# Kernel tuning notes

Measured on AMD Instinct MI355X. Metric: run time of the kernel, lower is better.

The kernel has to match this reference:

```python
import jax, jax.numpy as jnp
import numpy as np

N_NODES = 100000
N_EDGES = 3200000
IN_F, HID, OUT = 24, 64, 1


def _gcn_conv(x, W, b, src, dst, norm, n):
    # x: [N, Fin] -> h: [N, Fout]; PyG GCNConv: lin first, then normalized aggregation, then bias
    h = x @ W                                    # [N, Fout]
    msg = h[src] * norm[:, None]                 # [E+N, Fout] gathered, norm-weighted messages
    agg = jax.ops.segment_sum(msg, dst, num_segments=n)  # scatter-add to targets
    return agg + b


def setup_inputs() -> dict:
    key = jax.random.key(0)
    k1, k2, k3, k4 = jax.random.split(key, 4)
    x = jax.random.normal(k1, (N_NODES, IN_F), dtype=jnp.float32)
    edge_index = jax.random.randint(k2, (2, N_EDGES), 0, N_NODES, dtype=jnp.int64)
    # Glorot-ish init for weights
    W1 = jax.random.normal(k3, (IN_F, HID), dtype=jnp.float32) / np.sqrt(IN_F)
    b1 = jnp.zeros((HID,), dtype=jnp.float32)
    W2 = jax.random.normal(k4, (HID, OUT), dtype=jnp.float32) / np.sqrt(HID)
    b2 = jnp.zeros((OUT,), dtype=jnp.float32)
    return {"x": x, "edge_index": edge_index, "W1": W1, "b1": b1, "W2": W2, "b2": b2}


def reference(x, edge_index, W1, b1, W2, b2):
    n = x.shape[0]
    # add self-loops (PyG GCNConv default)
    loops = jnp.arange(n, dtype=edge_index.dtype)
    src = jnp.concatenate([edge_index[0], loops])
    dst = jnp.concatenate([edge_index[1], loops])
    # symmetric normalization: deg over targets of A+I, norm_e = d^-1/2[src] * d^-1/2[dst]
    deg = jax.ops.segment_sum(jnp.ones_like(dst, dtype=x.dtype), dst, num_segments=n)
    dinv = jnp.where(deg > 0, jax.lax.rsqrt(deg), 0.0)
    norm = dinv[src] * dinv[dst]
    h = _gcn_conv(x, W1, b1, src, dst, norm, n)
    h = jax.nn.relu(h)
    # F.dropout with training=self.training -> identity in eval mode (reference runs eval)
    out = _gcn_conv(h, W2, b2, src, dst, norm, n)
    return out
```

## Files before the change

kernel.cpp:

```cpp
#include <hip/hip_runtime.h>
#include <hip/hip_fp16.h>

#define IN_F 24
#define HID 64
#define NB 512
#define NPB 256
#define GSZ_MAX 256
#define PBUF 7168
#define SRC_BITS 17

typedef unsigned int u32;

__device__ __forceinline__ int bucket_lo(int b, int n) {
    return (int)(((long long)b * n + NB - 1) / NB);
}

__global__ __launch_bounds__(1024) void k_pcount(const int* __restrict__ dst,
                                                 u32* __restrict__ pc, int e, int n) {
    __shared__ u32 h[NB];
    for (int j = threadIdx.x; j < NB; j += 1024) h[j] = 0;
    __syncthreads();
    int blk = blockIdx.x;
    long long begin = (long long)e * blk / NPB;
    long long end   = (long long)e * (blk + 1) / NPB;
    for (long long i = begin + threadIdx.x; i < end; i += 1024) {
        int k = (int)((long long)dst[i] * NB / n);
        atomicAdd(&h[k], 1u);
    }
    __syncthreads();
    for (int j = threadIdx.x; j < NB; j += 1024) pc[(size_t)blk * NB + j] = h[j];
}

__global__ __launch_bounds__(256) void k_pscan_a(u32* __restrict__ pc,
                                                 u32* __restrict__ colsum) {
    __shared__ u32 ps[256];
    int t = blockIdx.x;
    int tid = threadIdx.x;
    u32 v = pc[(size_t)tid * NB + t];
    ps[tid] = v;
    __syncthreads();
    for (int off = 1; off < 256; off <<= 1) {
        u32 v2 = (tid >= off) ? ps[tid - off] : 0;
        __syncthreads();
        ps[tid] += v2;
        __syncthreads();
    }
    pc[(size_t)tid * NB + t] = ps[tid] - v;
    if (tid == 255) colsum[t] = ps[255];
}

__global__ void k_pscan_b(const u32* __restrict__ colsum, u32* __restrict__ basep) {
    __shared__ u32 s[NB];
    int t = threadIdx.x;
    u32 v = colsum[t];
    s[t] = v;
    __syncthreads();
    for (int off = 1; off < NB; off <<= 1) {
        u32 v2 = (t >= off) ? s[t - off] : 0;
        __syncthreads();
        s[t] += v2;
        __syncthreads();
    }
    basep[t] = s[t] - v;
}

__global__ __launch_bounds__(1024) void k_part(const int* __restrict__ src,
                                               const int* __restrict__ dst,
                                               const u32* __restrict__ pc,
                                               const u32* __restrict__ basep,
                                               u32* __restrict__ pairs, int e, int n) {
    __shared__ u32 cur[NB];
    int blk = (blockIdx.x & 7) * (NPB / 8) + (blockIdx.x >> 3);
    for (int j = threadIdx.x; j < NB; j += 1024)
        cur[j] = pc[(size_t)blk * NB + j] + basep[j];
    __syncthreads();
    long long begin = (long long)e * blk / NPB;
    long long end   = (long long)e * (blk + 1) / NPB;
    for (long long i = begin + threadIdx.x; i < end; i += 1024) {
        int d = dst[i];
        int sv = src[i];
        int k = (int)((long long)d * NB / n);
        u32 loc = (u32)(d - bucket_lo(k, n));
        u32 pos = atomicAdd(&cur[k], 1u);
        pairs[pos] = (loc << SRC_BITS) | (u32)sv;
    }
}

__global__ __launch_bounds__(512) void k_bucket(const u32* __restrict__ pairs,
                                                const u32* __restrict__ basep,
                                                const float* __restrict__ x,
                                                int* __restrict__ cnt,
                                                int* __restrict__ row_start,
                                                float* __restrict__ dinv,
                                                int* __restrict__ csr_src,
                                                __half2* __restrict__ xs2, int e, int n) {
    __shared__ u32 pbuf[PBUF];
    __shared__ u32 h[GSZ_MAX];
    __shared__ u32 cur[GSZ_MAX];
    __shared__ u32 sc[GSZ_MAX];
    __shared__ float dloc[GSZ_MAX];
    int b = blockIdx.x;
    if (b == 0 && threadIdx.x < 12)
        xs2[(long long)n * 12 + threadIdx.x] = __floats2half2_rn(0.0f, 0.0f);
    int lo = bucket_lo(b, n);
    int hi = bucket_lo(b + 1, n);
    int gsz = hi - lo;
    u32 start = basep[b];
    u32 endp = (b + 1 < NB) ? basep[b + 1] : (u32)e;
    int nbp = (int)(endp - start);
    for (int j = threadIdx.x; j < GSZ_MAX; j += 512) h[j] = 0;
    __syncthreads();
    int stored = nbp < PBUF ? nbp : PBUF;
    for (int i = threadIdx.x; i < stored; i += 512) {
        u32 p = pairs[start + i];
        pbuf[i] = p;
        atomicAdd(&h[p >> SRC_BITS], 1u);
    }
    for (int i = PBUF + threadIdx.x; i < nbp; i += 512) {
        atomicAdd(&h[pairs[start + i] >> SRC_BITS], 1u);
    }
    __syncthreads();
    int t = threadIdx.x;
    u32 v = 0;
    if (t < GSZ_MAX) { v = h[t]; sc[t] = v; }
    __syncthreads();
    for (int off = 1; off < GSZ_MAX; off <<= 1) {
        u32 v2 = (t >= off && t < GSZ_MAX) ? sc[t - off] : 0;
        __syncthreads();
        if (t < GSZ_MAX) sc[t] += v2;
        __syncthreads();
    }
    u32 excl = (t < GSZ_MAX) ? (sc[t] - v) : 0;
    if (t < gsz) {
        float dv = rsqrtf((float)(v + 1));
        cnt[lo + t] = (int)v;
        row_start[lo + t] = (int)(start + excl);
        dinv[lo + t] = dv;
        dloc[t] = dv;
        cur[t] = excl;
    }
    __syncthreads();
    for (int i = threadIdx.x; i < stored; i += 512) {
        u32 p = pbuf[i];
        u32 pos = atomicAdd(&cur[p >> SRC_BITS], 1u);
        csr_src[start + pos] = (int)(p & ((1u << SRC_BITS) - 1));
    }
    for (int i = PBUF + threadIdx.x; i < nbp; i += 512) {
        u32 p = pairs[start + i];
        u32 pos = atomicAdd(&cur[p >> SRC_BITS], 1u);
        csr_src[start + pos] = (int)(p & ((1u << SRC_BITS) - 1));
    }
    const float2* xf = (const float2*)(x + (long long)lo * IN_F);
    for (int i = threadIdx.x; i < gsz * 12; i += 512) {
        float2 vv = xf[i];
        float dn = dloc[i / 12];
        xs2[(long long)lo * 12 + i] = __floats2half2_rn(vv.x * dn, vv.y * dn);
    }
}

__global__ __launch_bounds__(256) void k_agg_hz(const float* __restrict__ x,
                                                const __half2* __restrict__ xs2,
                                                const float* __restrict__ dinv,
                                                const int* __restrict__ row_start,
                                                const int* __restrict__ cnt,
                                                const int* __restrict__ csr_src,
                                                const float* __restrict__ W1,
                                                const float* __restrict__ b1,
                                                const float* __restrict__ W2,
                                                float* __restrict__ zs, int n) {
    __shared__ float w[IN_F * HID];
    __shared__ float w2s[HID];
    __shared__ float b1s[HID];
    for (int j = threadIdx.x; j < IN_F * HID; j += 256) w[j] = W1[j];
    if (threadIdx.x < HID) { w2s[threadIdx.x] = W2[threadIdx.x]; b1s[threadIdx.x] = b1[threadIdx.x]; }
    __syncthreads();
    int g = threadIdx.x >> 3;
    int f4 = threadIdx.x & 7;
    int node = blockIdx.x * 32 + g;
    if (node >= n) return;
    float dn = dinv[node];
    const uint2* xq = (const uint2*)xs2;
    float ax0 = 0.0f, ay0 = 0.0f, ax1 = 0.0f, ay1 = 0.0f;
    if (f4 < 6) {
        int row = row_start[node];
        int c = cnt[node];
        float a0 = 0.0f, b0 = 0.0f, c0 = 0.0f, d0 = 0.0f;
        float a1 = 0.0f, b1v = 0.0f, c1 = 0.0f, d1 = 0.0f;
        int j = 0;
        for (; j + 16 <= c; j += 16) {
            const int* cp = csr_src + row + j;
            int s[16];
#pragma unroll
            for (int t = 0; t < 16; ++t) s[t] = cp[t];
            uint2 u[16];
#pragma unroll
            for (int t = 0; t < 16; ++t) u[t] = xq[(size_t)((u32)s[t] * 6u + (u32)f4)];
#pragma unroll
            for (int t = 0; t < 16; t += 2) {
                float2 e0 = __half22float2(__builtin_bit_cast(__half2, u[t].x));
                float2 e1 = __half22float2(__builtin_bit_cast(__half2, u[t].y));
                float2 o0 = __half22float2(__builtin_bit_cast(__half2, u[t + 1].x));
                float2 o1 = __half22float2(__builtin_bit_cast(__half2, u[t + 1].y));
                a0 += e0.x; b0 += e0.y; c0 += e1.x; d0 += e1.y;
                a1 += o0.x; b1v += o0.y; c1 += o1.x; d1 += o1.y;
            }
        }
        if (j < c) {
            const int* cp = csr_src + row + j;
            int rem = c - j;
            int s[16];
#pragma unroll
            for (int t = 0; t < 16; ++t) {
                int tmp = cp[t];
                s[t] = (t < rem) ? tmp : n;
            }
            uint2 u[16];
#pragma unroll
            for (int t = 0; t < 16; ++t) u[t] = xq[(size_t)((u32)s[t] * 6u + (u32)f4)];
#pragma unroll
            for (int t = 0; t < 16; t += 2) {
                float2 e0 = __half22float2(__builtin_bit_cast(__half2, u[t].x));
                float2 e1 = __half22float2(__builtin_bit_cast(__half2, u[t].y));
                float2 o0 = __half22float2(__builtin_bit_cast(__half2, u[t + 1].x));
                float2 o1 = __half22float2(__builtin_bit_cast(__half2, u[t + 1].y));
                a0 += e0.x; b0 += e0.y; c0 += e1.x; d0 += e1.y;
                a1 += o0.x; b1v += o0.y; c1 += o1.x; d1 += o1.y;
            }
        }
        ax0 = a0 + a1; ay0 = b0 + b1v; ax1 = c0 + c1; ay1 = d0 + d1;
        float4 sx4 = *(const float4*)(x + (long long)node * IN_F + 4 * f4);
        ax0 = (ax0 + sx4.x * dn) * dn;
        ay0 = (ay0 + sx4.y * dn) * dn;
        ax1 = (ax1 + sx4.z * dn) * dn;
        ay1 = (ay1 + sx4.w * dn) * dn;
    }
    int fb = f4 * 8;
    float h[8];
#pragma unroll
    for (int jj = 0; jj < 8; ++jj) h[jj] = b1s[fb + jj];
#pragma unroll
    for (int k = 0; k < IN_F; ++k) {
        int sl = k >> 2;
        int r = k & 3;
        float xv;
        if (r == 0)      xv = __shfl(ax0, sl, 8);
        else if (r == 1) xv = __shfl(ay0, sl, 8);
        else if (r == 2) xv = __shfl(ax1, sl, 8);
        else             xv = __shfl(ay1, sl, 8);
        const float* wr = w + k * HID + fb;
#pragma unroll
        for (int jj = 0; jj < 8; ++jj) h[jj] += xv * wr[jj];
    }
    float p = 0.0f;
#pragma unroll
    for (int jj = 0; jj < 8; ++jj) p += fmaxf(h[jj], 0.0f) * w2s[fb + jj];
    p += __shfl_down(p, 4, 8);
    p += __shfl_down(p, 2, 8);
    p += __shfl_down(p, 1, 8);
    if (f4 == 0) zs[node] = p * dn;
}

__global__ void k_out(const float* __restrict__ zs, const float* __restrict__ dinv,
                      const int* __restrict__ row_start, const int* __restrict__ cnt,
                      const int* __restrict__ csr_src, const float* __restrict__ b2,
                      float* __restrict__ out, int n) {
    int t = blockIdx.x * blockDim.x + threadIdx.x;
    int node = t >> 4;
    int lane = t & 15;
    if (node >= n) return;
    int row = row_start[node];
    int c = cnt[node];
    float v = 0.0f;
    for (int j = lane; j < c; j += 16) {
        v += zs[csr_src[row + j]];
    }
    v += __shfl_down(v, 8, 16);
    v += __shfl_down(v, 4, 16);
    v += __shfl_down(v, 2, 16);
    v += __shfl_down(v, 1, 16);
    if (lane == 0) {
        out[node] = b2[0] + dinv[node] * (zs[node] + v);
    }
}

extern "C" void kernel_launch(void* const* d_in, const int* in_sizes, int n_in,
                              void* d_out, int out_size, void* d_ws, size_t ws_size,
                              hipStream_t stream) {
    const float* x   = (const float*)d_in[0];
    const int*   ei  = (const int*)d_in[1];
    const float* W1  = (const float*)d_in[2];
    const float* b1  = (const float*)d_in[3];
    const float* W2  = (const float*)d_in[4];
    const float* b2  = (const float*)d_in[5];
    float* out = (float*)d_out;

    const int n = in_sizes[0] / IN_F;
    const int e = in_sizes[1] / 2;
    const int* src = ei;
    const int* dst = ei + e;

    const int B = 256;

    char* base = (char*)d_ws;
    u32* pairs     = (u32*)base;
    float* zs      = (float*)base;
    size_t ov = ((size_t)e * 4 + 255) & ~(size_t)255;
    char* after    = base + ov;
    int* cnt       = (int*)after;
    int* row_start = cnt + n;
    int* csr_src   = row_start + n;
    float* dinv    = (float*)(csr_src + e);
    __half* xs     = (__half*)(dinv + n);
    u32* pc        = (u32*)(xs + (size_t)(n + 1) * IN_F);
    u32* colsum    = pc + (size_t)NPB * NB;
    u32* basep     = colsum + NB;

    k_pcount<<<NPB, 1024, 0, stream>>>(dst, pc, e, n);
    k_pscan_a<<<NB, B, 0, stream>>>(pc, colsum);
    k_pscan_b<<<1, NB, 0, stream>>>(colsum, basep);
    k_part<<<NPB, 1024, 0, stream>>>(src, dst, pc, basep, pairs, e, n);
    k_bucket<<<NB, 512, 0, stream>>>(pairs, basep, x, cnt, row_start, dinv, csr_src,
                                     (__half2*)xs, e, n);

    k_agg_hz<<<(n + 31) / 32, B, 0, stream>>>(x, (const __half2*)xs, dinv,
                                              row_start, cnt, csr_src,
                                              W1, b1, W2, zs, n);

    const long long n16 = (long long)n * 16;
    k_out<<<(int)((n16 + B - 1) / B), B, 0, stream>>>(zs, dinv, row_start, cnt, csr_src, b2, out, n);
}
```

Before: 195.4 us.

## Replace two-level bucket partition CSR build with global atomic histogram and scatter

Replaces the bucketed two-pass partition (per-block bucket histograms, partition into pairs, then per-bucket local sort in shared memory) with a direct CSR build. The new build uses a global per-node atomic histogram, a three-kernel prefix scan, and a global atomic scatter of source indices. This drops the intermediate pairs buffer and one full pass over the edges. In exchange it relies on random global atomics over 100k counters, and rows are filled in nondeterministic order with poor write locality.

```diff
diff --git a/kernel.cpp b/kernel.cpp
--- a/kernel.cpp
+++ b/kernel.cpp
@@ -3,158 +3,115 @@
 
 #define IN_F 24
 #define HID 64
-#define NB 512
-#define NPB 256
-#define GSZ_MAX 256
-#define PBUF 7168
-#define SRC_BITS 17
+#define BLKN 1024
 
 typedef unsigned int u32;
 
-__device__ __forceinline__ int bucket_lo(int b, int n) {
-    return (int)(((long long)b * n + NB - 1) / NB);
-}
-
-__global__ __launch_bounds__(1024) void k_pcount(const int* __restrict__ dst,
-                                                 u32* __restrict__ pc, int e, int n) {
-    __shared__ u32 h[NB];
-    for (int j = threadIdx.x; j < NB; j += 1024) h[j] = 0;
-    __syncthreads();
-    int blk = blockIdx.x;
-    long long begin = (long long)e * blk / NPB;
-    long long end   = (long long)e * (blk + 1) / NPB;
-    for (long long i = begin + threadIdx.x; i < end; i += 1024) {
-        int k = (int)((long long)dst[i] * NB / n);
-        atomicAdd(&h[k], 1u);
-    }
-    __syncthreads();
-    for (int j = threadIdx.x; j < NB; j += 1024) pc[(size_t)blk * NB + j] = h[j];
-}
-
-__global__ __launch_bounds__(256) void k_pscan_a(u32* __restrict__ pc,
-                                                 u32* __restrict__ colsum) {
-    __shared__ u32 ps[256];
-    int t = blockIdx.x;
-    int tid = threadIdx.x;
-    u32 v = pc[(size_t)tid * NB + t];
-    ps[tid] = v;
+
+__global__ __launch_bounds__(1024) void k_hist(const int* __restrict__ dst,
+                                               u32* __restrict__ cnt, int e) {
+    int i = blockIdx.x * 1024 + threadIdx.x;
+    if (i < e) atomicAdd(&cnt[dst[i]], 1u);
+}
+
+__global__ __launch_bounds__(256) void k_scan_a(const u32* __restrict__ cnt,
+                                                u32* __restrict__ rs,
+                                                u32* __restrict__ bsum, int n) {
+    __shared__ u32 s[256];
+    int b = blockIdx.x;
+    int t = threadIdx.x;
+    int base = b * BLKN + t * 4;
+    u32 c0 = 0, c1 = 0, c2 = 0, c3 = 0;
+    if (base + 3 < n) {
+        uint4 v = *(const uint4*)(cnt + base);
+        c0 = v.x; c1 = v.y; c2 = v.z; c3 = v.w;
+    } else {
+        if (base + 0 < n) c0 = cnt[base + 0];
+        if (base + 1 < n) c1 = cnt[base + 1];
+        if (base + 2 < n) c2 = cnt[base + 2];
+        if (base + 3 < n) c3 = cnt[base + 3];
+    }
+    u32 tsum = c0 + c1 + c2 + c3;
+    s[t] = tsum;
     __syncthreads();
     for (int off = 1; off < 256; off <<= 1) {
-        u32 v2 = (tid >= off) ? ps[tid - off] : 0;
-        __syncthreads();
-        ps[tid] += v2;
-        __syncthreads();
-    }
-    pc[(size_t)tid * NB + t] = ps[tid] - v;
-    if (tid == 255) colsum[t] = ps[255];
-}
-
-__global__ void k_pscan_b(const u32* __restrict__ colsum, u32* __restrict__ basep) {
-    __shared__ u32 s[NB];
+        u32 v2 = (t >= off) ? s[t - off] : 0;
+        __syncthreads();
+        s[t] += v2;
+        __syncthreads();
+    }
+    u32 excl = s[t] - tsum;
+    u32 p0 = excl, p1 = excl + c0, p2 = p1 + c1, p3 = p2 + c2;
+    if (base + 3 < n) {
+        *(uint4*)(rs + base) = make_uint4(p0, p1, p2, p3);
+    } else {
+        if (base + 0 < n) rs[base + 0] = p0;
+        if (base + 1 < n) rs[base + 1] = p1;
+        if (base + 2 < n) rs[base + 2] = p2;
+        if (base + 3 < n) rs[base + 3] = p3;
+    }
+    if (t == 255) bsum[b] = s[255];
+}
+
+__global__ void k_scan_b(u32* __restrict__ bsum, int nb) {
+    __shared__ u32 s[128];
     int t = threadIdx.x;
-    u32 v = colsum[t];
+    u32 v = (t < nb) ? bsum[t] : 0;
     s[t] = v;
     __syncthreads();
-    for (int off = 1; off < NB; off <<= 1) {
+    for (int off = 1; off < 128; off <<= 1) {
         u32 v2 = (t >= off) ? s[t - off] : 0;
         __syncthreads();
         s[t] += v2;
         __syncthreads();
     }
-    basep[t] = s[t] - v;
-}
-
-__global__ __launch_bounds__(1024) void k_part(const int* __restrict__ src,
-                                               const int* __restrict__ dst,
-                                               const u32* __restrict__ pc,
-                                               const u32* __restrict__ basep,
-                                               u32* __restrict__ pairs, int e, int n) {
-    __shared__ u32 cur[NB];
-    int blk = (blockIdx.x & 7) * (NPB / 8) + (blockIdx.x >> 3);
-    for (int j = threadIdx.x; j < NB; j += 1024)
-        cur[j] = pc[(size_t)blk * NB + j] + basep[j];
-    __syncthreads();
-    long long begin = (long long)e * blk / NPB;
-    long long end   = (long long)e * (blk + 1) / NPB;
-    for (long long i = begin + threadIdx.x; i < end; i += 1024) {
-        int d = dst[i];
-        int sv = src[i];
-        int k = (int)((long long)d * NB / n);
-        u32 loc = (u32)(d - bucket_lo(k, n));
-        u32 pos = atomicAdd(&cur[k], 1u);
-        pairs[pos] = (loc << SRC_BITS) | (u32)sv;
-    }
-}
-
-__global__ __launch_bounds__(512) void k_bucket(const u32* __restrict__ pairs,
-                                                const u32* __restrict__ basep,
+    if (t < nb) bsum[t] = s[t] - v;
+}
+
+__global__ __launch_bounds__(256) void k_scan_c(const u32* __restrict__ cnt,
+                                                u32* __restrict__ rs,
+                                                const u32* __restrict__ bsum,
+                                                u32* __restrict__ cur,
+                                                float* __restrict__ dinv,
                                                 const float* __restrict__ x,
-                                                int* __restrict__ cnt,
-                                                int* __restrict__ row_start,
-                                                float* __restrict__ dinv,
-                                                int* __restrict__ csr_src,
-                                                __half2* __restrict__ xs2, int e, int n) {
-    __shared__ u32 pbuf[PBUF];
-    __shared__ u32 h[GSZ_MAX];
-    __shared__ u32 cur[GSZ_MAX];
-    __shared__ u32 sc[GSZ_MAX];
-    __shared__ float dloc[GSZ_MAX];
+                                                __half2* __restrict__ xs2, int n) {
+    __shared__ float dloc[BLKN];
     int b = blockIdx.x;
-    if (b == 0 && threadIdx.x < 12)
-        xs2[(long long)n * 12 + threadIdx.x] = __floats2half2_rn(0.0f, 0.0f);
-    int lo = bucket_lo(b, n);
-    int hi = bucket_lo(b + 1, n);
-    int gsz = hi - lo;
-    u32 start = basep[b];
-    u32 endp = (b + 1 < NB) ? basep[b + 1] : (u32)e;
-    int nbp = (int)(endp - start);
-    for (int j = threadIdx.x; j < GSZ_MAX; j += 512) h[j] = 0;
-    __syncthreads();
-    int stored = nbp < PBUF ? nbp : PBUF;
-    for (int i = threadIdx.x; i < stored; i += 512) {
-        u32 p = pairs[start + i];
-        pbuf[i] = p;
-        atomicAdd(&h[p >> SRC_BITS], 1u);
-    }
-    for (int i = PBUF + threadIdx.x; i < nbp; i += 512) {
-        atomicAdd(&h[pairs[start + i] >> SRC_BITS], 1u);
-    }
-    __syncthreads();
-    int t = threadIdx.x;
-    u32 v = 0;
-    if (t < GSZ_MAX) { v = h[t]; sc[t] = v; }
-    __syncthreads();
-    for (int off = 1; off < GSZ_MAX; off <<= 1) {
-        u32 v2 = (t >= off && t < GSZ_MAX) ? sc[t - off] : 0;
-        __syncthreads();
-        if (t < GSZ_MAX) sc[t] += v2;
-        __syncthreads();
-    }
-    u32 excl = (t < GSZ_MAX) ? (sc[t] - v) : 0;
-    if (t < gsz) {
-        float dv = rsqrtf((float)(v + 1));
-        cnt[lo + t] = (int)v;
-        row_start[lo + t] = (int)(start + excl);
-        dinv[lo + t] = dv;
-        dloc[t] = dv;
-        cur[t] = excl;
-    }
-    __syncthreads();
-    for (int i = threadIdx.x; i < stored; i += 512) {
-        u32 p = pbuf[i];
-        u32 pos = atomicAdd(&cur[p >> SRC_BITS], 1u);
-        csr_src[start + pos] = (int)(p & ((1u << SRC_BITS) - 1));
-    }
-    for (int i = PBUF + threadIdx.x; i < nbp; i += 512) {
-        u32 p = pairs[start + i];
-        u32 pos = atomicAdd(&cur[p >> SRC_BITS], 1u);
-        csr_src[start + pos] = (int)(p & ((1u << SRC_BITS) - 1));
-    }
+    u32 off = bsum[b];
+    int lo = b * BLKN;
+    int cnt_here = n - lo;
+    if (cnt_here > BLKN) cnt_here = BLKN;
+    for (int i = threadIdx.x; i < cnt_here; i += 256) {
+        int node = lo + i;
+        u32 r = rs[node] + off;
+        rs[node] = r;
+        cur[node] = r;
+        float dv = rsqrtf((float)(cnt[node] + 1));
+        dinv[node] = dv;
+        dloc[i] = dv;
+    }
+    __syncthreads();
     const float2* xf = (const float2*)(x + (long long)lo * IN_F);
-    for (int i = threadIdx.x; i < gsz * 12; i += 512) {
+    int tot = cnt_here * 12;
+    for (int i = threadIdx.x; i < tot; i += 256) {
         float2 vv = xf[i];
         float dn = dloc[i / 12];
         xs2[(long long)lo * 12 + i] = __floats2half2_rn(vv.x * dn, vv.y * dn);
+    }
+    if (b == 0 && threadIdx.x < 12)
+        xs2[(long long)n * 12 + threadIdx.x] = __floats2half2_rn(0.0f, 0.0f);
+}
+
+__global__ __launch_bounds__(1024) void k_scatter(const int* __restrict__ src,
+                                                  const int* __restrict__ dst,
+                                                  u32* __restrict__ cur,
+                                                  int* __restrict__ csr_src, int e) {
+    int i = blockIdx.x * 1024 + threadIdx.x;
+    if (i < e) {
+        int d = dst[i];
+        int s = src[i];
+        u32 pos = atomicAdd(&cur[d], 1u);
+        csr_src[pos] = s;
     }
 }
 
@@ -299,33 +256,31 @@
     const int* src = ei;
     const int* dst = ei + e;
 
-    const int B = 256;
-
     char* base = (char*)d_ws;
-    u32* pairs     = (u32*)base;
-    float* zs      = (float*)base;
-    size_t ov = ((size_t)e * 4 + 255) & ~(size_t)255;
-    char* after    = base + ov;
-    int* cnt       = (int*)after;
-    int* row_start = cnt + n;
-    int* csr_src   = row_start + n;
-    float* dinv    = (float*)(csr_src + e);
-    __half* xs     = (__half*)(dinv + n);
-    u32* pc        = (u32*)(xs + (size_t)(n + 1) * IN_F);
-    u32* colsum    = pc + (size_t)NPB * NB;
-    u32* basep     = colsum + NB;
-
-    k_pcount<<<NPB, 1024, 0, stream>>>(dst, pc, e, n);
-    k_pscan_a<<<NB, B, 0, stream>>>(pc, colsum);
-    k_pscan_b<<<1, NB, 0, stream>>>(colsum, basep);
-    k_part<<<NPB, 1024, 0, stream>>>(src, dst, pc, basep, pairs, e, n);
-    k_bucket<<<NB, 512, 0, stream>>>(pairs, basep, x, cnt, row_start, dinv, csr_src,
-                                     (__half2*)xs, e, n);
-
-    k_agg_hz<<<(n + 31) / 32, B, 0, stream>>>(x, (const __half2*)xs, dinv,
-                                              row_start, cnt, csr_src,
-                                              W1, b1, W2, zs, n);
+    u32* cnt       = (u32*)base;
+    u32* cur       = cnt + n;
+    u32* row_start = cur + n;
+    float* dinv    = (float*)(row_start + n);
+    float* zs      = dinv + n;
+    u32* bsum      = (u32*)(zs + n);
+    int* csr_src   = (int*)(bsum + 128);
+    __half* xs     = (__half*)(csr_src + e);
+
+    const int nscan = (n + BLKN - 1) / BLKN;
+
+    hipMemsetAsync(cnt, 0, (size_t)n * sizeof(u32), stream);
+    k_hist<<<(e + 1023) / 1024, 1024, 0, stream>>>(dst, cnt, e);
+    k_scan_a<<<nscan, 256, 0, stream>>>(cnt, row_start, bsum, n);
+    k_scan_b<<<1, 128, 0, stream>>>(bsum, nscan);
+    k_scan_c<<<nscan, 256, 0, stream>>>(cnt, row_start, bsum, cur, dinv, x,
+                                        (__half2*)xs, n);
+    k_scatter<<<(e + 1023) / 1024, 1024, 0, stream>>>(src, dst, cur, csr_src, e);
+
+    k_agg_hz<<<(n + 31) / 32, 256, 0, stream>>>(x, (const __half2*)xs, dinv,
+                                                (const int*)row_start, (const int*)cnt,
+                                                csr_src, W1, b1, W2, zs, n);
 
     const long long n16 = (long long)n * 16;
-    k_out<<<(int)((n16 + B - 1) / B), B, 0, stream>>>(zs, dinv, row_start, cnt, csr_src, b2, out, n);
-}
+    k_out<<<(int)((n16 + 255) / 256), 256, 0, stream>>>(zs, dinv, (const int*)row_start,
+                                                        (const int*)cnt, csr_src, b2, out, n);
+}
```

After: 560.4 us. 2.87x slower.
